# Performance work log

Measured on AMD Instinct MI355X. Metric: run time of the kernel, lower is better.

Reference implementation:

```python
import jax, jax.numpy as jnp
import numpy as np

N, E = 50000, 800000
IN_C, HID, HEADS, OUT_C = 128, 64, 4, 64
NEG_SLOPE = 0.2


def _gat_layer(x, src, dst, W, a_src, a_dst, b, heads, out_dim, concat):
    n = x.shape[0]
    h = (x @ W).reshape(n, heads, out_dim)                      # [N,H,D]
    s_src = jnp.einsum('nhd,hd->nh', h, a_src)                  # [N,H]
    s_dst = jnp.einsum('nhd,hd->nh', h, a_dst)
    e = jax.nn.leaky_relu(s_src[src] + s_dst[dst], NEG_SLOPE)   # [Etot,H]
    m = jax.ops.segment_max(e, dst, num_segments=n)             # per-dst max (self-loops => no empty segments)
    w = jnp.exp(e - m[dst])
    denom = jax.ops.segment_sum(w, dst, num_segments=n)
    alpha = w / denom[dst]                                      # segment softmax over incoming edges
    msg = h[src] * alpha[..., None]                             # [Etot,H,D] edge gather + weight
    out = jax.ops.segment_sum(msg, dst, num_segments=n)         # scatter-sum aggregate
    out = out.reshape(n, heads * out_dim) if concat else out.mean(axis=1)
    return out + b


def setup_inputs() -> dict:
    key = jax.random.key(0)
    ks = jax.random.split(key, 10)
    x = jax.random.normal(ks[0], (N, IN_C), dtype=jnp.float32)
    edge_index = jax.random.randint(ks[1], (2, E), 0, N, dtype=jnp.int64)
    s1 = 1.0 / np.sqrt(IN_C)
    s2 = 1.0 / np.sqrt(HID * HEADS)
    return {
        'x': x,
        'edge_index': edge_index,
        'W1': jax.random.normal(ks[2], (IN_C, HEADS * HID), dtype=jnp.float32) * s1,
        'a_src1': jax.random.normal(ks[3], (HEADS, HID), dtype=jnp.float32) * s1,
        'a_dst1': jax.random.normal(ks[4], (HEADS, HID), dtype=jnp.float32) * s1,
        'b1': jnp.zeros((HEADS * HID,), dtype=jnp.float32),
        'W2': jax.random.normal(ks[5], (HEADS * HID, OUT_C), dtype=jnp.float32) * s2,
        'a_src2': jax.random.normal(ks[6], (1, OUT_C), dtype=jnp.float32) * s2,
        'a_dst2': jax.random.normal(ks[7], (1, OUT_C), dtype=jnp.float32) * s2,
        'b2': jnp.zeros((OUT_C,), dtype=jnp.float32),
    }


def reference(x, edge_index, W1, a_src1, a_dst1, b1, W2, a_src2, a_dst2, b2):
    n = x.shape[0]
    loop = jnp.arange(n, dtype=edge_index.dtype)
    src = jnp.concatenate([edge_index[0], loop])  # PyG GATConv adds self-loops
    dst = jnp.concatenate([edge_index[1], loop])
    # dropout layers are identity in eval mode
    h = _gat_layer(x, src, dst, W1, a_src1, a_dst1, b1, HEADS, HID, concat=True)
    h = jax.nn.elu(h)
    h = _gat_layer(h, src, dst, W2, a_src2, a_dst2, b2, 1, OUT_C, concat=False)
    return jnp.min(h, axis=0)
```

## Files before the change

### kernel.cpp

```cpp
#include <hip/hip_runtime.h>
#include <math.h>

typedef unsigned short ushort_t;
typedef __attribute__((ext_vector_type(8))) short bf16x8;
typedef __attribute__((ext_vector_type(4))) float f32x4;


__device__ inline unsigned fenc(float f) {
    unsigned u = __float_as_uint(f);
    return (u & 0x80000000u) ? ~u : (u | 0x80000000u);
}
__device__ inline float fdec(unsigned u) {
    return __uint_as_float((u & 0x80000000u) ? (u ^ 0x80000000u) : ~u);
}

__device__ inline float wrsum(float v) {
    #pragma unroll
    for (int m = 32; m; m >>= 1) v += __shfl_xor(v, m, 64);
    return v;
}
__device__ inline float lrelu(float x) { return x > 0.f ? x : 0.2f * x; }

__device__ inline ushort_t f2bf(float f) {
    unsigned u = __float_as_uint(f);
    u += 0x7FFFu + ((u >> 16) & 1u);
    return (ushort_t)(u >> 16);
}
__device__ inline float bflo(unsigned u) { return __uint_as_float(u << 16); }
__device__ inline float bfhi(unsigned u) { return __uint_as_float(u & 0xFFFF0000u); }

__global__ __launch_bounds__(256) void pre_kernel(const float* __restrict__ W1,
                                                  const float* __restrict__ W2,
                                                  const float* __restrict__ a_src2,
                                                  const float* __restrict__ a_dst2,
                                                  ushort_t* __restrict__ W1s,
                                                  ushort_t* __restrict__ W2s,
                                                  float* __restrict__ va,
                                                  float* __restrict__ vb) {
    int bid = blockIdx.x;
    int tid = threadIdx.x;
    if (bid < 128) {
        int idx = bid * 256 + tid;
        int j = idx & 7;
        int lane = (idx >> 3) & 63;
        int ct = (idx >> 9) & 15;
        int kc = (idx >> 13) & 3;
        int k = kc * 32 + (lane >> 4) * 8 + j;
        int c = ct * 16 + (lane & 15);
        W1s[idx] = f2bf(W1[k * 256 + c]);
    } else if (bid < 192) {
        int idx = (bid - 128) * 256 + tid;
        int j = idx & 7;
        int lane = (idx >> 3) & 63;
        int ct = (idx >> 9) & 3;
        int kc = idx >> 11;
        int k = kc * 32 + (lane >> 4) * 8 + j;
        int c = ct * 16 + (lane & 15);
        W2s[idx] = f2bf(W2[k * 64 + c]);
    } else {
        int k = tid;
        float sa = 0.f, sb = 0.f;
        #pragma unroll 8
        for (int c = 0; c < 64; c++) {
            float w = W2[k * 64 + c];
            sa += w * a_src2[c];
            sb += w * a_dst2[c];
        }
        va[k] = sa;
        vb[k] = sb;
    }
}

__global__ __launch_bounds__(256) void front_kernel(const float* __restrict__ x,
                                                    const ushort_t* __restrict__ W1s,
                                                    const float* __restrict__ a_src,
                                                    const float* __restrict__ a_dst,
                                                    ushort_t* __restrict__ h1b,
                                                    float* __restrict__ ssrc,
                                                    float* __restrict__ sdst,
                                                    const int* __restrict__ ei,
                                                    int* __restrict__ deg,
                                                    int* __restrict__ rankb,
                                                    int N, int E, int Etot, int nb16) {
    __shared__ float ss[16 * 257];
    __shared__ float ps[256];
    int bid = blockIdx.x;
    int tid = threadIdx.x;

    if (bid >= nb16) {
        int i = (bid - nb16) * 256 + tid;
        if (i < Etot) {
            int d = (i < E) ? ei[E + i] : (i - E);
            rankb[i] = atomicAdd(&deg[d], 1);
        }
        return;
    }

    int base = bid * 16;
    int lane = tid & 63, wv = tid >> 6;
    int m = lane & 15, q = lane >> 4;

    bool rowok = (base + m) < N;
    bf16x8 afrag[4];
    #pragma unroll
    for (int kc = 0; kc < 4; kc++) {
        float4 xa = make_float4(0.f, 0.f, 0.f, 0.f), xb = xa;
        if (rowok) {
            const float* xp = x + (size_t)(base + m) * 128 + kc * 32 + q * 8;
            xa = *(const float4*)xp;
            xb = *(const float4*)(xp + 4);
        }
        bf16x8 af;
        af[0] = (short)f2bf(xa.x); af[1] = (short)f2bf(xa.y);
        af[2] = (short)f2bf(xa.z); af[3] = (short)f2bf(xa.w);
        af[4] = (short)f2bf(xb.x); af[5] = (short)f2bf(xb.y);
        af[6] = (short)f2bf(xb.z); af[7] = (short)f2bf(xb.w);
        afrag[kc] = af;
    }

    #pragma unroll
    for (int t = 0; t < 4; t++) {
        int ct = wv * 4 + t;
        f32x4 acc = {0.f, 0.f, 0.f, 0.f};
        #pragma unroll
        for (int kc = 0; kc < 4; kc++) {
            bf16x8 bfrag = *(const bf16x8*)(W1s + (((size_t)(kc * 16 + ct) * 64 + lane) << 3));
            acc = __builtin_amdgcn_mfma_f32_16x16x32_bf16(afrag[kc], bfrag, acc, 0, 0, 0);
        }
        #pragma unroll
        for (int reg = 0; reg < 4; reg++) {
            ss[(q * 4 + reg) * 257 + ct * 16 + m] = acc[reg];
        }
    }
    __syncthreads();

    int dd = tid & 63, hh = tid >> 6;
    #pragma unroll
    for (int j = 0; j < 16; j++) {
        int n = base + j;
        if (n < N) h1b[(size_t)n * 256 + dd * 4 + hh] = f2bf(ss[j * 257 + tid]);
    }
    int j = tid & 15, hh2 = (tid >> 4) & 3, which = (tid >> 6) & 1, half = tid >> 7;
    const float* av = which ? a_dst : a_src;
    int cbase = hh2 * 64 + half * 32;
    float sum = 0.f;
    #pragma unroll
    for (int i = 0; i < 32; i++) {
        int ii = (i + 8 * hh2) & 31;
        sum += ss[j * 257 + cbase + ii] * av[cbase + ii];
    }
    ps[tid] = sum;
    __syncthreads();
    if (half == 0) {
        float tot = sum + ps[tid + 128];
        int n = base + j;
        if (n < N) (which ? sdst : ssrc)[n * 4 + hh2] = tot;
    }
}

__global__ __launch_bounds__(256) void chunksum_kernel(const int* __restrict__ deg,
                                                       int* __restrict__ csum, int M) {
    __shared__ int sm[256];
    int t = blockIdx.x * 256 + threadIdx.x;
    sm[threadIdx.x] = (t < M) ? deg[t] : 0;
    __syncthreads();
    for (int off = 128; off > 0; off >>= 1) {
        if (threadIdx.x < off) sm[threadIdx.x] += sm[threadIdx.x + off];
        __syncthreads();
    }
    if (threadIdx.x == 0) csum[blockIdx.x] = sm[0];
}

__global__ __launch_bounds__(256) void scanchunks_kernel(const int* __restrict__ csum,
                                                         int* __restrict__ coffset, int nchunks) {
    __shared__ int sm[256];
    int v = (threadIdx.x < nchunks) ? csum[threadIdx.x] : 0;
    sm[threadIdx.x] = v;
    __syncthreads();
    for (int off = 1; off < 256; off <<= 1) {
        int a = (threadIdx.x >= off) ? sm[threadIdx.x - off] : 0;
        __syncthreads();
        sm[threadIdx.x] += a;
        __syncthreads();
    }
    coffset[threadIdx.x] = sm[threadIdx.x] - v;
}

__global__ __launch_bounds__(256) void rowptr_kernel(const int* __restrict__ deg,
                                                     const int* __restrict__ coffset,
                                                     int* __restrict__ rowptr, int M) {
    __shared__ int sm[256];
    int t = blockIdx.x * 256 + threadIdx.x;
    int v = (t < M) ? deg[t] : 0;
    sm[threadIdx.x] = v;
    __syncthreads();
    for (int off = 1; off < 256; off <<= 1) {
        int a = (threadIdx.x >= off) ? sm[threadIdx.x - off] : 0;
        __syncthreads();
        sm[threadIdx.x] += a;
        __syncthreads();
    }
    if (t < M) rowptr[t] = coffset[blockIdx.x] + sm[threadIdx.x] - v;
}

__global__ __launch_bounds__(256) void scatter_kernel(const int* __restrict__ ei,
                                                      const int* __restrict__ rowptr,
                                                      const int* __restrict__ rankb,
                                                      int* __restrict__ srcbuf, int E, int Etot) {
    int i = blockIdx.x * 256 + threadIdx.x;
    if (i >= Etot) return;
    int s, d;
    if (i < E) { s = ei[i]; d = ei[E + i]; } else { s = d = i - E; }
    srcbuf[rowptr[d] + rankb[i]] = s;
}

__global__ __launch_bounds__(256) void agg1_kernel(const int* __restrict__ rowptr,
                                                   const int* __restrict__ srcbuf,
                                                   const float* __restrict__ ssrc,
                                                   const float* __restrict__ sdst,
                                                   const ushort_t* __restrict__ h1b,
                                                   const float* __restrict__ b1,
                                                   const float* __restrict__ va,
                                                   const float* __restrict__ vb,
                                                   ushort_t* __restrict__ x2b,
                                                   float* __restrict__ ssrc2,
                                                   float* __restrict__ sdst2, int N) {
    __shared__ int    s_sh[4][64];
    __shared__ float4 w_sh[4][64];
    int lane = threadIdx.x & 63, w = threadIdx.x >> 6;
    int d = blockIdx.x * 4 + w;
    if (d >= N) return;
    int row = rowptr[d], end = rowptr[d + 1];
    float4 sd = *(const float4*)(sdst + d * 4);
    float l0 = 0.f, l1 = 0.f, l2 = 0.f, l3 = 0.f;
    float a0 = 0.f, a1 = 0.f, a2 = 0.f, a3 = 0.f;

    for (int base = row; base < end; base += 64) {
        int cnt = min(64, end - base);
        bool valid = lane < cnt;
        int s = valid ? srcbuf[base + lane] : 0;
        float4 ssv = *(const float4*)(ssrc + s * 4);
        float w0 = valid ? __expf(lrelu(ssv.x + sd.x)) : 0.f;
        float w1 = valid ? __expf(lrelu(ssv.y + sd.y)) : 0.f;
        float w2 = valid ? __expf(lrelu(ssv.z + sd.z)) : 0.f;
        float w3 = valid ? __expf(lrelu(ssv.w + sd.w)) : 0.f;
        l0 += wrsum(w0);  l1 += wrsum(w1);
        l2 += wrsum(w2);  l3 += wrsum(w3);
        s_sh[w][lane] = s;
        w_sh[w][lane] = make_float4(w0, w1, w2, w3);
        int cnt4 = (cnt + 3) & ~3;
        for (int j = 0; j < cnt4; j += 4) {
            int sj0 = s_sh[w][j], sj1 = s_sh[w][j + 1], sj2 = s_sh[w][j + 2], sj3 = s_sh[w][j + 3];
            float4 wj0 = w_sh[w][j], wj1 = w_sh[w][j + 1], wj2 = w_sh[w][j + 2], wj3 = w_sh[w][j + 3];
            uint2 u0 = *(const uint2*)(h1b + (size_t)sj0 * 256 + lane * 4);
            uint2 u1 = *(const uint2*)(h1b + (size_t)sj1 * 256 + lane * 4);
            uint2 u2 = *(const uint2*)(h1b + (size_t)sj2 * 256 + lane * 4);
            uint2 u3 = *(const uint2*)(h1b + (size_t)sj3 * 256 + lane * 4);
            a0 += wj0.x * bflo(u0.x); a1 += wj0.y * bfhi(u0.x);
            a2 += wj0.z * bflo(u0.y); a3 += wj0.w * bfhi(u0.y);
            a0 += wj1.x * bflo(u1.x); a1 += wj1.y * bfhi(u1.x);
            a2 += wj1.z * bflo(u1.y); a3 += wj1.w * bfhi(u1.y);
            a0 += wj2.x * bflo(u2.x); a1 += wj2.y * bfhi(u2.x);
            a2 += wj2.z * bflo(u2.y); a3 += wj2.w * bfhi(u2.y);
            a0 += wj3.x * bflo(u3.x); a1 += wj3.y * bfhi(u3.x);
            a2 += wj3.z * bflo(u3.y); a3 += wj3.w * bfhi(u3.y);
        }
    }
    float v0 = a0 / l0 + b1[lane];
    float v1 = a1 / l1 + b1[64 + lane];
    float v2 = a2 / l2 + b1[128 + lane];
    float v3 = a3 / l3 + b1[192 + lane];
    v0 = v0 > 0.f ? v0 : __expf(v0) - 1.f;
    v1 = v1 > 0.f ? v1 : __expf(v1) - 1.f;
    v2 = v2 > 0.f ? v2 : __expf(v2) - 1.f;
    v3 = v3 > 0.f ? v3 : __expf(v3) - 1.f;
    ushort_t* xp = x2b + (size_t)d * 256;
    xp[lane] = f2bf(v0); xp[64 + lane] = f2bf(v1);
    xp[128 + lane] = f2bf(v2); xp[192 + lane] = f2bf(v3);
    float sa = v0 * va[lane] + v1 * va[64 + lane] + v2 * va[128 + lane] + v3 * va[192 + lane];
    float sb = v0 * vb[lane] + v1 * vb[64 + lane] + v2 * vb[128 + lane] + v3 * vb[192 + lane];
    sa = wrsum(sa);
    sb = wrsum(sb);
    if (lane == 0) { ssrc2[d] = sa; sdst2[d] = sb; }
}

__global__ __launch_bounds__(256) void gemmz_kernel(const ushort_t* __restrict__ x2b,
                                                    const ushort_t* __restrict__ W2s,
                                                    const float* __restrict__ b2,
                                                    float* __restrict__ z, int N) {
    int base = blockIdx.x * 32;
    int tid = threadIdx.x;
    int lane = tid & 63, wv = tid >> 6;
    int m = lane & 15, q = lane >> 4;
    int c = wv * 16 + m;
    float bc = b2[c];

    #pragma unroll
    for (int h = 0; h < 2; h++) {
        int rbase = base + h * 16;
        bool rowok = (rbase + m) < N;
        const ushort_t* xrow = x2b + (size_t)(rbase + m) * 256;
        f32x4 acc = {0.f, 0.f, 0.f, 0.f};
        #pragma unroll
        for (int kc = 0; kc < 8; kc++) {
            bf16x8 af = {0, 0, 0, 0, 0, 0, 0, 0};
            if (rowok) af = *(const bf16x8*)(xrow + kc * 32 + q * 8);
            bf16x8 bf = *(const bf16x8*)(W2s + (((size_t)(kc * 4 + wv) * 64 + lane) << 3));
            acc = __builtin_amdgcn_mfma_f32_16x16x32_bf16(af, bf, acc, 0, 0, 0);
        }
        #pragma unroll
        for (int reg = 0; reg < 4; reg++) {
            int n = rbase + q * 4 + reg;
            if (n < N) z[(size_t)n * 64 + c] = acc[reg] + bc;
        }
    }
}

__global__ __launch_bounds__(256) void aggz_kernel(const int* __restrict__ rowptr,
                                                   const int* __restrict__ srcbuf,
                                                   const float* __restrict__ ssrc,
                                                   const float* __restrict__ sdst,
                                                   const float* __restrict__ z,
                                                   unsigned* __restrict__ minenc, int N) {
    __shared__ int   s_sh[4][64];
    __shared__ float w_sh[4][64];
    __shared__ float sm[256];
    int lane = threadIdx.x & 63, w = threadIdx.x >> 6;
    float minv = INFINITY;

    for (int d0 = blockIdx.x * 4; d0 < N; d0 += gridDim.x * 4) {
        int d = d0 + w;
        if (d < N) {
            int row = rowptr[d], end = rowptr[d + 1];
            float sdv = sdst[d];
            float l = 0.f;
            float a0 = 0.f, a1 = 0.f, a2 = 0.f, a3 = 0.f;
            for (int base = row; base < end; base += 64) {
                int cnt = min(64, end - base);
                bool valid = lane < cnt;
                int s = valid ? srcbuf[base + lane] : 0;
                float wt = valid ? __expf(lrelu(ssrc[s] + sdv)) : 0.f;
                l += wrsum(wt);
                s_sh[w][lane] = s;
                w_sh[w][lane] = wt;
                int cnt4 = (cnt + 3) & ~3;
                for (int j = 0; j < cnt4; j += 4) {
                    int sj0 = s_sh[w][j], sj1 = s_sh[w][j + 1];
                    int sj2 = s_sh[w][j + 2], sj3 = s_sh[w][j + 3];
                    float wj0 = w_sh[w][j], wj1 = w_sh[w][j + 1];
                    float wj2 = w_sh[w][j + 2], wj3 = w_sh[w][j + 3];
                    float z0 = z[(size_t)sj0 * 64 + lane];
                    float z1 = z[(size_t)sj1 * 64 + lane];
                    float z2 = z[(size_t)sj2 * 64 + lane];
                    float z3 = z[(size_t)sj3 * 64 + lane];
                    a0 += wj0 * z0; a1 += wj1 * z1;
                    a2 += wj2 * z2; a3 += wj3 * z3;
                }
            }
            float out = ((a0 + a1) + (a2 + a3)) / l;
            minv = fminf(minv, out);
        }
    }
    sm[threadIdx.x] = minv;
    __syncthreads();
    if (w == 0) {
        float v = fminf(fminf(sm[lane], sm[64 + lane]), fminf(sm[128 + lane], sm[192 + lane]));
        atomicMin(&minenc[lane], fenc(v));
    }
}

__global__ void decode_kernel(const unsigned* __restrict__ minenc, float* __restrict__ out) {
    int d = threadIdx.x;
    if (d < 64) out[d] = fdec(minenc[d]);
}

extern "C" void kernel_launch(void* const* d_in, const int* in_sizes, int n_in,
                              void* d_out, int out_size, void* d_ws, size_t ws_size,
                              hipStream_t stream) {
    const float* x      = (const float*)d_in[0];
    const int*   ei     = (const int*)d_in[1];
    const float* W1     = (const float*)d_in[2];
    const float* a_src1 = (const float*)d_in[3];
    const float* a_dst1 = (const float*)d_in[4];
    const float* b1     = (const float*)d_in[5];
    const float* W2     = (const float*)d_in[6];
    const float* a_src2 = (const float*)d_in[7];
    const float* a_dst2 = (const float*)d_in[8];
    const float* b2     = (const float*)d_in[9];
    float* out = (float*)d_out;

    const int N = in_sizes[0] / 128;
    const int E = in_sizes[1] / 2;
    const int Etot = E + N;
    const int Epad = Etot + 64;
    const int M = N + 1;
    const int nchunks = (M + 255) / 256;

    float* ws = (float*)d_ws;
    ushort_t* h1b = (ushort_t*)ws;
    ushort_t* x2b = (ushort_t*)(ws + (size_t)N * 128);
    float* z      = ws + (size_t)N * 256;
    ushort_t* W1s = (ushort_t*)(ws + (size_t)N * 320);
    ushort_t* W2s = (ushort_t*)(ws + (size_t)N * 320 + 16384);
    float* ssrc1  = ws + (size_t)N * 320 + 24576;
    float* sdst1  = ssrc1 + (size_t)N * 4;
    float* ssrc2  = sdst1 + (size_t)N * 4;
    float* sdst2  = ssrc2 + N;
    float* va     = sdst2 + N;
    float* vb     = va + 256;
    int*   deg    = (int*)(vb + 256);
    int*   rowptr = deg + M;
    int*   csum   = rowptr + M;
    int*   coff   = csum + 256;
    int*   srcbuf = coff + 256;
    int*   rankb  = srcbuf + Epad;
    unsigned* minenc = (unsigned*)(rankb + Epad);

    hipMemsetAsync(deg, 0, (size_t)M * 4, stream);
    hipMemsetAsync(minenc, 0xFF, 64 * 4, stream);

    int nb16 = (N + 15) / 16;
    int nb32 = (N + 31) / 32;
    int nb4 = (N + 3) / 4;
    int nbh = (Etot + 255) / 256;
    int nbz = 1568;

    pre_kernel<<<193, 256, 0, stream>>>(W1, W2, a_src2, a_dst2, W1s, W2s, va, vb);
    front_kernel<<<nb16 + nbh, 256, 0, stream>>>(x, W1s, a_src1, a_dst1, h1b, ssrc1, sdst1,
                                                 ei, deg, rankb, N, E, Etot, nb16);

    chunksum_kernel<<<nchunks, 256, 0, stream>>>(deg, csum, M);
    scanchunks_kernel<<<1, 256, 0, stream>>>(csum, coff, nchunks);
    rowptr_kernel<<<nchunks, 256, 0, stream>>>(deg, coff, rowptr, M);
    scatter_kernel<<<(Etot + 255) / 256, 256, 0, stream>>>(ei, rowptr, rankb, srcbuf, E, Etot);

    agg1_kernel<<<nb4, 256, 0, stream>>>(rowptr, srcbuf, ssrc1, sdst1, h1b, b1,
                                         va, vb, x2b, ssrc2, sdst2, N);
    gemmz_kernel<<<nb32, 256, 0, stream>>>(x2b, W2s, b2, z, N);
    aggz_kernel<<<nbz, 256, 0, stream>>>(rowptr, srcbuf, ssrc2, sdst2, z, minenc, N);
    decode_kernel<<<1, 64, 0, stream>>>(minenc, out);
}
```

Before: 311.6 us.

## Fold memsets into pre kernel, stage x via LDS, vectorize h1b stores

Removes the two hipMemsetAsync launches by zeroing deg and initializing minenc inside extra blocks of pre_kernel. In front_kernel, x rows are first loaded coalesced into padded shared memory before building the MFMA A fragments, which adds a barrier. The h1b write-out now packs four bf16 values into a single 8-byte store per thread instead of issuing 2-byte scattered stores. The aim is to cut launch overhead and improve global memory coalescing.

```diff
diff --git a/kernel.cpp b/kernel.cpp
--- a/kernel.cpp
+++ b/kernel.cpp
@@ -36,7 +36,10 @@
                                                   ushort_t* __restrict__ W1s,
                                                   ushort_t* __restrict__ W2s,
                                                   float* __restrict__ va,
-                                                  float* __restrict__ vb) {
+                                                  float* __restrict__ vb,
+                                                  int* __restrict__ deg,
+                                                  unsigned* __restrict__ minenc,
+                                                  int M) {
     int bid = blockIdx.x;
     int tid = threadIdx.x;
     if (bid < 128) {
@@ -57,7 +60,7 @@
         int k = kc * 32 + (lane >> 4) * 8 + j;
         int c = ct * 16 + (lane & 15);
         W2s[idx] = f2bf(W2[k * 64 + c]);
-    } else {
+    } else if (bid == 192) {
         int k = tid;
         float sa = 0.f, sb = 0.f;
         #pragma unroll 8
@@ -68,6 +71,10 @@
         }
         va[k] = sa;
         vb[k] = sb;
+        if (tid < 64) minenc[tid] = 0xFFFFFFFFu;
+    } else {
+        int t = (bid - 193) * 256 + tid;
+        if (t < M) deg[t] = 0;
     }
 }
 
@@ -97,19 +104,26 @@
     }
 
     int base = bid * 16;
+    {
+        const float4* xv = (const float4*)(x + (size_t)base * 128);
+        float4* xs4 = (float4*)ss;
+        #pragma unroll
+        for (int i = tid; i < 512; i += 256) {
+            int row = i >> 5;
+            float4 v = (base + row < N) ? xv[i] : make_float4(0.f, 0.f, 0.f, 0.f);
+            xs4[row * 33 + (i & 31)] = v;
+        }
+    }
+    __syncthreads();
+
     int lane = tid & 63, wv = tid >> 6;
     int m = lane & 15, q = lane >> 4;
-
-    bool rowok = (base + m) < N;
     bf16x8 afrag[4];
     #pragma unroll
     for (int kc = 0; kc < 4; kc++) {
-        float4 xa = make_float4(0.f, 0.f, 0.f, 0.f), xb = xa;
-        if (rowok) {
-            const float* xp = x + (size_t)(base + m) * 128 + kc * 32 + q * 8;
-            xa = *(const float4*)xp;
-            xb = *(const float4*)(xp + 4);
-        }
+        const float* xp = ss + m * 132 + kc * 32 + q * 8;
+        float4 xa = *(const float4*)xp;
+        float4 xb = *(const float4*)(xp + 4);
         bf16x8 af;
         af[0] = (short)f2bf(xa.x); af[1] = (short)f2bf(xa.y);
         af[2] = (short)f2bf(xa.z); af[3] = (short)f2bf(xa.w);
@@ -117,6 +131,7 @@
         af[6] = (short)f2bf(xb.z); af[7] = (short)f2bf(xb.w);
         afrag[kc] = af;
     }
+    __syncthreads();
 
     #pragma unroll
     for (int t = 0; t < 4; t++) {
@@ -134,11 +149,17 @@
     }
     __syncthreads();
 
-    int dd = tid & 63, hh = tid >> 6;
-    #pragma unroll
-    for (int j = 0; j < 16; j++) {
+    int dd = tid & 63, jj = tid >> 6;
+    #pragma unroll
+    for (int t2 = 0; t2 < 4; t2++) {
+        int j = jj + t2 * 4;
         int n = base + j;
-        if (n < N) h1b[(size_t)n * 256 + dd * 4 + hh] = f2bf(ss[j * 257 + tid]);
+        if (n < N) {
+            const float* row = ss + j * 257;
+            unsigned p0 = (unsigned)f2bf(row[dd]) | ((unsigned)f2bf(row[64 + dd]) << 16);
+            unsigned p1 = (unsigned)f2bf(row[128 + dd]) | ((unsigned)f2bf(row[192 + dd]) << 16);
+            *(uint2*)(h1b + (size_t)n * 256 + dd * 4) = make_uint2(p0, p1);
+        }
     }
     int j = tid & 15, hh2 = (tid >> 4) & 3, which = (tid >> 6) & 1, half = tid >> 7;
     const float* av = which ? a_dst : a_src;
@@ -416,16 +437,15 @@
     int*   rankb  = srcbuf + Epad;
     unsigned* minenc = (unsigned*)(rankb + Epad);
 
-    hipMemsetAsync(deg, 0, (size_t)M * 4, stream);
-    hipMemsetAsync(minenc, 0xFF, 64 * 4, stream);
-
     int nb16 = (N + 15) / 16;
     int nb32 = (N + 31) / 32;
     int nb4 = (N + 3) / 4;
     int nbh = (Etot + 255) / 256;
     int nbz = 1568;
-
-    pre_kernel<<<193, 256, 0, stream>>>(W1, W2, a_src2, a_dst2, W1s, W2s, va, vb);
+    int nbdeg = (M + 255) / 256;
+
+    pre_kernel<<<193 + nbdeg, 256, 0, stream>>>(W1, W2, a_src2, a_dst2, W1s, W2s,
+                                                va, vb, deg, minenc, M);
     front_kernel<<<nb16 + nbh, 256, 0, stream>>>(x, W1s, a_src1, a_dst1, h1b, ssrc1, sdst1,
                                                  ei, deg, rankb, N, E, Etot, nb16);
 
```

Measured after the change: 290.8 us. 6.7% less time.
